# Optimization experiments

Hardware: AMD Instinct MI355X
Metric: run time of the kernel (lower is better)

Reference implementation:

```python
import jax, jax.numpy as jnp
import numpy as np
import math


def setup_inputs() -> dict:
    key = jax.random.key(0)
    ks = jax.random.split(key, 8)
    B, C, H, W = 8, 512, 48, 48
    Cq = C // 8
    s = 0.05
    return {
        "x": jax.random.normal(ks[0], (B, C, H, W), jnp.float32),
        "Wq": jax.random.normal(ks[1], (Cq, C), jnp.float32) * s,
        "bq": jax.random.normal(ks[2], (Cq,), jnp.float32) * s,
        "Wk": jax.random.normal(ks[3], (Cq, C), jnp.float32) * s,
        "bk": jax.random.normal(ks[4], (Cq,), jnp.float32) * s,
        "Wv": jax.random.normal(ks[5], (C, C), jnp.float32) * s,
        "bv": jax.random.normal(ks[6], (C,), jnp.float32) * s,
        "gamma": jax.random.normal(ks[7], (1,), jnp.float32),
    }


def reference(x, Wq, bq, Wk, bk, Wv, bv, gamma):
    B, C, H, W = x.shape
    Cq = Wq.shape[0]
    N = H * W
    xf = x.reshape(B, C, N)  # 1x1 conv == channel matmul
    q = jnp.einsum('oc,bcn->bno', Wq, xf) + bq  # [B, N, Cq] (proj_query, permuted)
    k = jnp.einsum('oc,bcn->bon', Wk, xf) + bk[None, :, None]  # [B, Cq, N]
    v = jnp.einsum('oc,bcn->bon', Wv, xf) + bv[None, :, None]  # [B, C, N]
    # ave_I = (1/Cq)*(I - (1/Cq)*J); Q @ ave_I = (Q - rowmean(Q)) / Cq
    qc = (q - jnp.mean(q, axis=-1, keepdims=True)) / Cq
    sigma = jnp.einsum('bnc,bcm->bnm', qc, k) / math.sqrt(Cq)  # [B, N, N]
    attention = jax.nn.softmax(sigma, axis=-1)
    # out = V @ attention^T : out[b,c,n] = sum_m v[b,c,m] * attention[b,n,m]
    am = jnp.einsum('bcm,bnm->bcn', v, attention).reshape(B, C, H, W)
    out = gamma[0] * am + x
    return out
```

## Files before the change

### kernel.cpp

```cpp
#include <hip/hip_runtime.h>

#define B_ 8
#define C_ 512
#define N_ 2304
#define CQ 64

typedef float f32x2 __attribute__((ext_vector_type(2)));
typedef float f32x4 __attribute__((ext_vector_type(4)));
typedef float f32x16 __attribute__((ext_vector_type(16)));
typedef short bf16x8 __attribute__((ext_vector_type(8)));
typedef unsigned short u16x4 __attribute__((ext_vector_type(4)));
typedef unsigned short u16x8 __attribute__((ext_vector_type(8)));
typedef int i32x4 __attribute__((ext_vector_type(4)));

__device__ __forceinline__ unsigned short f2bf(float f){
  union { float f; unsigned int u; } v; v.f = f;
  unsigned int r = (v.u + 0x7fffu + ((v.u >> 16) & 1u)) >> 16;
  return (unsigned short)r;
}

__device__ __forceinline__ void gload_lds16(const void* g, void* l){
  __builtin_amdgcn_global_load_lds(
      (const __attribute__((address_space(1))) unsigned int*)g,
      (__attribute__((address_space(3))) unsigned int*)l, 16, 0, 0);
}

__device__ __forceinline__ void fp8q_to_bf16(int w0, int w1, bf16x8* o){
  f32x2 a = __builtin_amdgcn_cvt_pk_f32_fp8(w0, false);
  f32x2 b = __builtin_amdgcn_cvt_pk_f32_fp8(w0, true);
  f32x2 c = __builtin_amdgcn_cvt_pk_f32_fp8(w1, false);
  f32x2 d = __builtin_amdgcn_cvt_pk_f32_fp8(w1, true);
  unsigned int u0,u1,u2,u3;
  asm("v_cvt_pk_bf16_f32 %0, %1, %2" : "=v"(u0) : "v"(a[0]), "v"(a[1]));
  asm("v_cvt_pk_bf16_f32 %0, %1, %2" : "=v"(u1) : "v"(b[0]), "v"(b[1]));
  asm("v_cvt_pk_bf16_f32 %0, %1, %2" : "=v"(u2) : "v"(c[0]), "v"(c[1]));
  asm("v_cvt_pk_bf16_f32 %0, %1, %2" : "=v"(u3) : "v"(d[0]), "v"(d[1]));
  union { unsigned int u[4]; bf16x8 v; } r;
  r.u[0]=u0; r.u[1]=u1; r.u[2]=u2; r.u[3]=u3;
  *o = r.v;
}

__global__ __launch_bounds__(256) void k_wcvt(const float* __restrict__ Wq,
                                              const float* __restrict__ Wk,
                                              const float* __restrict__ Wv,
                                              unsigned short* __restrict__ Wb){
  int idx = blockIdx.x*256 + threadIdx.x;
  int h = idx & 1, ln = (idx >> 1) & 31, cs = (idx >> 6) & 31, ob = idx >> 11;
  int row = ob*32 + ln, col = cs*16 + h*8;
  const float* src;
  if (row < 64)       src = Wq + (size_t)row*512 + col;
  else if (row < 128) src = Wk + (size_t)(row-64)*512 + col;
  else                src = Wv + (size_t)(row-128)*512 + col;
  f32x4 v0 = *(const f32x4*)src;
  f32x4 v1 = *(const f32x4*)(src + 4);
  u16x8 o;
  #pragma unroll
  for (int j = 0; j < 4; j++){ o[j] = f2bf(v0[j]); o[4+j] = f2bf(v1[j]); }
  *(u16x8*)(Wb + (size_t)idx*8) = o;
}

__global__ __launch_bounds__(512) void k_prep(const float* __restrict__ x,
                                              const float* __restrict__ bq,
                                              const float* __restrict__ bk,
                                              const float* __restrict__ bv,
                                              const unsigned short* __restrict__ Wb,
                                              unsigned short* __restrict__ qw,
                                              unsigned short* __restrict__ kw,
                                              unsigned short* __restrict__ vw){
  __shared__ short xt_l[32*520];
  __shared__ float scr[2*32*68];

  int i = blockIdx.x; int b = i & 7; int nt = i >> 3;
  int n0 = nt*32;
  int t = threadIdx.x; int w = t >> 6; int l = t & 63;
  int h = l >> 5, ln = l & 31;
  const size_t bN = (size_t)b*N_;

  #pragma unroll
  for (int it = 0; it < 8; it++){
    int c = it*64 + (t >> 3);
    int n4 = (t & 7)*4;
    f32x4 v = *(const f32x4*)(x + ((size_t)b*C_ + c)*N_ + n0 + n4);
    #pragma unroll
    for (int j = 0; j < 4; j++) xt_l[(n4+j)*520 + c] = (short)f2bf(v[j]);
  }
  __syncthreads();

  const unsigned short* wlane = Wb + (size_t)(ln*2 + h)*8;
  const unsigned short* wv0 = wlane + (size_t)(4 + 2*w)*16384;
  const unsigned short* wv1 = wlane + (size_t)(5 + 2*w)*16384;
  const unsigned short* wqk = wlane + (size_t)w*16384;

  f32x16 vacc[2]; f32x16 qkacc;
  #pragma unroll
  for (int rr = 0; rr < 16; rr++){ vacc[0][rr]=0.f; vacc[1][rr]=0.f; qkacc[rr]=0.f; }

  #pragma unroll 8
  for (int cs = 0; cs < 32; cs++){
    bf16x8 bx = *(const bf16x8*)&xt_l[ln*520 + cs*16 + h*8];
    bf16x8 a0 = *(const bf16x8*)(wv0 + (size_t)cs*512);
    bf16x8 a1 = *(const bf16x8*)(wv1 + (size_t)cs*512);
    vacc[0] = __builtin_amdgcn_mfma_f32_32x32x16_bf16(a0, bx, vacc[0], 0, 0, 0);
    vacc[1] = __builtin_amdgcn_mfma_f32_32x32x16_bf16(a1, bx, vacc[1], 0, 0, 0);
    if (w < 4){
      bf16x8 aq = *(const bf16x8*)(wqk + (size_t)cs*512);
      qkacc = __builtin_amdgcn_mfma_f32_32x32x16_bf16(aq, bx, qkacc, 0, 0, 0);
    }
  }

  if (w < 4){
    float* s = scr + ((w >> 1) ? 2176 : 0);
    int obase = (w & 1)*32;
    #pragma unroll
    for (int rr = 0; rr < 16; rr++){
      int o = obase + (rr & 3) + 8*(rr >> 2) + 4*h;
      s[ln*68 + o] = qkacc[rr];
    }
  }
  __syncthreads();

  if (t < 256){
    int isK = t >> 7;
    int tt = t & 127;
    int n = tt >> 2, j = tt & 3;
    const float* s = scr + (isK ? 2176 : 0);
    const float* bias = isK ? bk : bq;
    float vals[16]; float sm = 0.f;
    #pragma unroll
    for (int ii = 0; ii < 16; ii++){
      vals[ii] = s[n*68 + j*16 + ii] + bias[j*16 + ii];
      sm += vals[ii];
    }
    sm += __shfl_xor(sm, 1); sm += __shfl_xor(sm, 2);
    float mean = isK ? 0.f : sm * (1.f/64.f);
    float scl  = isK ? 1.f : (1.44269504089f/512.f);
    u16x8 h0, h1;
    #pragma unroll
    for (int ii = 0; ii < 8; ii++) h0[ii] = f2bf((vals[ii]   - mean)*scl);
    #pragma unroll
    for (int ii = 0; ii < 8; ii++) h1[ii] = f2bf((vals[8+ii] - mean)*scl);
    unsigned short* d = (isK ? kw : qw) + (bN + n0 + n)*CQ + j*16;
    *(u16x8*)d = h0;
    *(u16x8*)(d + 8) = h1;
  }
  __syncthreads();

  #pragma unroll
  for (int r = 0; r < 4; r++){
    if ((w >> 1) == r){
      float* s = scr + (w & 1)*2176;
      #pragma unroll
      for (int of = 0; of < 2; of++)
        #pragma unroll
        for (int rr = 0; rr < 16; rr++){
          int o = of*32 + (rr & 3) + 8*(rr >> 2) + 4*h;
          s[ln*68 + o] = vacc[of][rr];
        }
    }
    __syncthreads();
    {
      int ch = t >> 8;
      int tt = t & 255;
      int o = tt >> 2, jj = (tt >> 1) & 1, half = tt & 1;
      int og = (2*r + ch)*64 + o;
      const float* s = scr + ch*2176;
      float bvv = bv[og];
      u16x8 hv;
      #pragma unroll
      for (int ii = 0; ii < 8; ii++){
        int q2 = ((ii & 3) | ((ii & 4) << 1)) + half*4;
        hv[ii] = f2bf(s[(jj*16 + q2)*68 + o] + bvv);
      }
      *(u16x8*)(vw + ((size_t)b*C_ + og)*N_ + n0 + jj*16 + half*8) = hv;
    }
    __syncthreads();
  }
}

__global__ __launch_bounds__(256) void k_sexp(const unsigned short* __restrict__ qw,
                                              const unsigned short* __restrict__ kw,
                                              unsigned char* __restrict__ Plf,
                                              float* __restrict__ lsum_part,
                                              int b0, int bsh){
  int bid = blockIdx.x;
  int bl = bid & ((1 << bsh) - 1);
  int b = b0 + bl;
  int r = bid >> bsh;
  int ms = r & 3; int nt = r >> 2;
  int t = threadIdx.x; int w = t >> 6; int l = t & 63;
  int h = l >> 5, ln = l & 31;
  int nf = w & 1, mh = w >> 1;
  int n = nt*64 + nf*32 + ln;

  const unsigned short* qb = qw + ((size_t)b*N_ + n)*CQ + h*8;
  bf16x8 qf[4];
  #pragma unroll
  for (int kq = 0; kq < 4; kq++) qf[kq] = *(const bf16x8*)(qb + kq*16);

  int mb32base = ms*18 + mh*9;
  const unsigned short* ks0 = kw + ((size_t)b*N_ + ln)*CQ + h*8 + (size_t)mb32base*32*CQ;
  unsigned char* pbf = Plf + (((size_t)bl*72*N_ + n)*32) + h*16;

  float lsum = 0.f;
  bf16x8 ka[4], kc[4];
  #pragma unroll
  for (int kq = 0; kq < 4; kq++) ka[kq] = *(const bf16x8*)(ks0 + kq*16);

  #define SEXP_BODY(MF, KF, KN, PFOFF)                                          \
  {                                                                             \
    _Pragma("unroll")                                                           \
    for (int kq = 0; kq < 4; kq++)                                              \
      KN[kq] = *(const bf16x8*)(ks0 + (size_t)(PFOFF)*32*CQ + kq*16);           \
    f32x16 sv;                                                                  \
    _Pragma("unroll")                                                           \
    for (int rr = 0; rr < 16; rr++) sv[rr] = 0.f;                               \
    _Pragma("unroll")                                                           \
    for (int kq = 0; kq < 4; kq++)                                              \
      sv = __builtin_amdgcn_mfma_f32_32x32x16_bf16(KF[kq], qf[kq], sv, 0, 0, 0);\
    float e[16];                                                                \
    _Pragma("unroll")                                                           \
    for (int rr = 0; rr < 16; rr++) e[rr] = exp2f(sv[rr]);                      \
    _Pragma("unroll")                                                           \
    for (int rr = 0; rr < 16; rr++) lsum += e[rr];                              \
    int w0 = __builtin_amdgcn_cvt_pk_fp8_f32(e[0],  e[1],  0,  false);          \
    w0     = __builtin_amdgcn_cvt_pk_fp8_f32(e[2],  e[3],  w0, true);           \
    int w1 = __builtin_amdgcn_cvt_pk_fp8_f32(e[4],  e[5],  0,  false);          \
    w1     = __builtin_amdgcn_cvt_pk_fp8_f32(e[6],  e[7],  w1, true);           \
    int w2 = __builtin_amdgcn_cvt_pk_fp8_f32(e[8],  e[9],  0,  false);          \
    w2     = __builtin_amdgcn_cvt_pk_fp8_f32(e[10], e[11], w2, true);           \
    int w3 = __builtin_amdgcn_cvt_pk_fp8_f32(e[12], e[13], 0,  false);          \
    w3     = __builtin_amdgcn_cvt_pk_fp8_f32(e[14], e[15], w3, true);           \
    i32x4 pk4 = (i32x4){w0, w1, w2, w3};                                        \
    *(i32x4*)(pbf + (size_t)(mb32base + (MF))*((size_t)N_*32)) = pk4;           \
  }

  #pragma unroll
  for (int it = 0; it < 4; it++){
    SEXP_BODY(2*it,     ka, kc, 2*it + 1)
    SEXP_BODY(2*it + 1, kc, ka, 2*it + 2)
  }
  SEXP_BODY(8, ka, kc, 8)
  #undef SEXP_BODY

  lsum += __shfl_xor(lsum, 32);
  if (l < 32)
    lsum_part[((size_t)bl*8 + ms*2 + mh)*N_ + n] = lsum;
}

__global__ __launch_bounds__(256, 1) void k_pv(const unsigned short* __restrict__ vw,
                                               const unsigned char* __restrict__ Plf,
                                               const float* __restrict__ lsum_part,
                                               const float* __restrict__ x,
                                               const float* __restrict__ gamma_p,
                                               float* __restrict__ out,
                                               int b0, int bsh){
  __shared__ __attribute__((aligned(16))) short At[3][128*64];

  int bid = blockIdx.x;
  int bl = bid & ((1 << bsh) - 1);
  int b = b0 + bl;
  int r = bid >> bsh;
  int cb = r & 3; int nb = r >> 2;
  int c0 = cb*128, n0g = nb*64;
  int t = threadIdx.x; int w = t >> 6; int l = t & 63;
  int h = l >> 5, ln = l & 31;
  int wc = w & 1, wn = w >> 1;

  int gc = ((l & 7) - (l >> 3)) & 7;
  const unsigned short* asrc0 = vw + ((size_t)b*C_ + c0 + w*32 + (l >> 3))*N_ + gc*8;
  int aro[2][4];
  #pragma unroll
  for (int cf = 0; cf < 2; cf++)
    #pragma unroll
    for (int mb = 0; mb < 4; mb++){
      int row = wc*64 + cf*32 + ln;
      aro[cf][mb] = (row*8 + ((mb*2 + h + row) & 7)) * 16;
    }
  const unsigned char* Pbf = Plf + (size_t)bl*72*N_*32;
  size_t pstep = (size_t)N_*32;
  size_t boffB = (size_t)(n0g + wn*32 + ln)*32 + h*16;

  f32x16 acc[2];
  #pragma unroll
  for (int cf = 0; cf < 2; cf++)
    #pragma unroll
    for (int rr = 0; rr < 16; rr++) acc[cf][rr] = 0.f;

  i32x4 B0[2], B1[2], B2[2];

  #pragma unroll
  for (int j = 0; j < 4; j++)
    gload_lds16(asrc0 + (size_t)j*8*N_, &At[0][w*2048 + j*512]);
  B0[0] = *(const i32x4*)(Pbf + boffB);
  B0[1] = *(const i32x4*)(Pbf + pstep + boffB);
  #pragma unroll
  for (int j = 0; j < 4; j++)
    gload_lds16(asrc0 + (size_t)j*8*N_ + 64, &At[1][w*2048 + j*512]);
  B1[0] = *(const i32x4*)(Pbf + 2*pstep + boffB);
  B1[1] = *(const i32x4*)(Pbf + 3*pstep + boffB);
  asm volatile("s_waitcnt vmcnt(8)" ::: "memory");
  __builtin_amdgcn_s_barrier();
  __builtin_amdgcn_sched_barrier(0);

  #define PV_STEP(KT, RD, WR, BC, BN)                                           \
  {                                                                             \
    const char* Ab = (const char*)At[RD];                                       \
    bf16x8 a_[2][4];                                                            \
    _Pragma("unroll")                                                           \
    for (int cf = 0; cf < 2; cf++)                                              \
      _Pragma("unroll")                                                         \
      for (int mb = 0; mb < 4; mb++)                                            \
        a_[cf][mb] = *(const bf16x8*)(Ab + aro[cf][mb]);                        \
    int m2 = ((KT) + 2 < 36) ? ((KT) + 2)*64 : 0;                               \
    _Pragma("unroll")                                                           \
    for (int j = 0; j < 4; j++)                                                 \
      gload_lds16(asrc0 + (size_t)j*8*N_ + m2, &At[WR][w*2048 + j*512]);        \
    {                                                                           \
      size_t pr2 = (size_t)((((KT) + 2 < 36) ? ((KT) + 2)*2 : 0));              \
      BN[0] = *(const i32x4*)(Pbf + pr2*pstep + boffB);                         \
      BN[1] = *(const i32x4*)(Pbf + (pr2 + 1)*pstep + boffB);                   \
    }                                                                           \
    bf16x8 bfr[4];                                                              \
    fp8q_to_bf16(BC[0][0], BC[0][1], &bfr[0]);                                  \
    fp8q_to_bf16(BC[0][2], BC[0][3], &bfr[1]);                                  \
    fp8q_to_bf16(BC[1][0], BC[1][1], &bfr[2]);                                  \
    fp8q_to_bf16(BC[1][2], BC[1][3], &bfr[3]);                                  \
    _Pragma("unroll")                                                           \
    for (int cf = 0; cf < 2; cf++)                                              \
      _Pragma("unroll")                                                         \
      for (int mb = 0; mb < 4; mb++)                                            \
        acc[cf] = __builtin_amdgcn_mfma_f32_32x32x16_bf16(                      \
            a_[cf][mb], bfr[mb], acc[cf], 0, 0, 0);                             \
    asm volatile("s_waitcnt vmcnt(8) lgkmcnt(0)" ::: "memory");                 \
    __builtin_amdgcn_s_barrier();                                               \
    __builtin_amdgcn_sched_barrier(0);                                          \
  }

  for (int it = 0; it < 6; it++){
    int kt = it*6;
    PV_STEP(kt+0, 0, 2, B0, B2)
    PV_STEP(kt+1, 1, 0, B1, B0)
    PV_STEP(kt+2, 2, 1, B2, B1)
    PV_STEP(kt+3, 0, 2, B0, B2)
    PV_STEP(kt+4, 1, 0, B1, B0)
    PV_STEP(kt+5, 2, 1, B2, B1)
  }
  #undef PV_STEP

  float gmv = gamma_p[0];
  {
    int n = n0g + wn*32 + ln;
    float s = 0.f;
    #pragma unroll
    for (int j = 0; j < 8; j++) s += lsum_part[((size_t)bl*8 + j)*N_ + n];
    float f = gmv / s;
    #pragma unroll
    for (int cf = 0; cf < 2; cf++){
      #pragma unroll
      for (int rr = 0; rr < 16; rr++){
        int c = c0 + wc*64 + cf*32 + (rr & 3) + 8*(rr >> 2) + 4*h;
        size_t idx = ((size_t)b*C_ + c)*N_ + n;
        out[idx] = acc[cf][rr]*f + x[idx];
      }
    }
  }
}

extern "C" void kernel_launch(void* const* d_in, const int* in_sizes, int n_in,
                              void* d_out, int out_size, void* d_ws, size_t ws_size,
                              hipStream_t stream) {
  (void)in_sizes; (void)n_in; (void)out_size;
  const float* x  = (const float*)d_in[0];
  const float* Wq = (const float*)d_in[1];
  const float* bq = (const float*)d_in[2];
  const float* Wk = (const float*)d_in[3];
  const float* bk = (const float*)d_in[4];
  const float* Wv = (const float*)d_in[5];
  const float* bv = (const float*)d_in[6];
  const float* gm = (const float*)d_in[7];
  float* out = (float*)d_out;

  const size_t qw_b = (size_t)B_*N_*CQ*2;
  const size_t vw_b = (size_t)B_*C_*N_*2;
  const size_t wb_b = (size_t)640*512*2;

  int nbg = 8, bsh = 3;
  for (;;){
    size_t pl_b   = (size_t)nbg*72*N_*32;
    size_t lsum_b = (size_t)nbg*8*N_*4;
    size_t need   = pl_b + 2*qw_b + vw_b + lsum_b + wb_b;
    if (need <= ws_size || nbg == 1) break;
    nbg >>= 1; bsh--;
  }
  size_t pl_b   = (size_t)nbg*72*N_*32;
  size_t lsum_b = (size_t)nbg*8*N_*4;

  char* wsc = (char*)d_ws;
  unsigned char* Plf = (unsigned char*)wsc;
  unsigned short* qw = (unsigned short*)(wsc + pl_b);
  unsigned short* kw = (unsigned short*)(wsc + pl_b + qw_b);
  unsigned short* vw = (unsigned short*)(wsc + pl_b + 2*qw_b);
  float* lsum_part   = (float*)(wsc + pl_b + 2*qw_b + vw_b);
  unsigned short* Wb = (unsigned short*)(wsc + pl_b + 2*qw_b + vw_b + lsum_b);

  k_wcvt<<<160, 256, 0, stream>>>(Wq, Wk, Wv, Wb);
  k_prep<<<576, 512, 0, stream>>>(x, bq, bk, bv, Wb, qw, kw, vw);

  for (int b0 = 0; b0 < B_; b0 += nbg){
    k_sexp<<<144*nbg, 256, 0, stream>>>(qw, kw, Plf, lsum_part, b0, bsh);
    k_pv<<<144*nbg, 256, 0, stream>>>(vw, Plf, lsum_part, x, gm, out, b0, bsh);
  }
}
```

Before: 121.4 us.

## Store V in fp8 and use fp8×fp8 MFMA for the PV product

```diff
diff --git a/kernel.cpp b/kernel.cpp
--- a/kernel.cpp
+++ b/kernel.cpp
@@ -11,6 +11,7 @@
 typedef short bf16x8 __attribute__((ext_vector_type(8)));
 typedef unsigned short u16x4 __attribute__((ext_vector_type(4)));
 typedef unsigned short u16x8 __attribute__((ext_vector_type(8)));
+typedef int i32x2 __attribute__((ext_vector_type(2)));
 typedef int i32x4 __attribute__((ext_vector_type(4)));
 
 __device__ __forceinline__ unsigned short f2bf(float f){
@@ -23,21 +24,6 @@
   __builtin_amdgcn_global_load_lds(
       (const __attribute__((address_space(1))) unsigned int*)g,
       (__attribute__((address_space(3))) unsigned int*)l, 16, 0, 0);
-}
-
-__device__ __forceinline__ void fp8q_to_bf16(int w0, int w1, bf16x8* o){
-  f32x2 a = __builtin_amdgcn_cvt_pk_f32_fp8(w0, false);
-  f32x2 b = __builtin_amdgcn_cvt_pk_f32_fp8(w0, true);
-  f32x2 c = __builtin_amdgcn_cvt_pk_f32_fp8(w1, false);
-  f32x2 d = __builtin_amdgcn_cvt_pk_f32_fp8(w1, true);
-  unsigned int u0,u1,u2,u3;
-  asm("v_cvt_pk_bf16_f32 %0, %1, %2" : "=v"(u0) : "v"(a[0]), "v"(a[1]));
-  asm("v_cvt_pk_bf16_f32 %0, %1, %2" : "=v"(u1) : "v"(b[0]), "v"(b[1]));
-  asm("v_cvt_pk_bf16_f32 %0, %1, %2" : "=v"(u2) : "v"(c[0]), "v"(c[1]));
-  asm("v_cvt_pk_bf16_f32 %0, %1, %2" : "=v"(u3) : "v"(d[0]), "v"(d[1]));
-  union { unsigned int u[4]; bf16x8 v; } r;
-  r.u[0]=u0; r.u[1]=u1; r.u[2]=u2; r.u[3]=u3;
-  *o = r.v;
 }
 
 __global__ __launch_bounds__(256) void k_wcvt(const float* __restrict__ Wq,
@@ -66,7 +52,7 @@
                                               const unsigned short* __restrict__ Wb,
                                               unsigned short* __restrict__ qw,
                                               unsigned short* __restrict__ kw,
-                                              unsigned short* __restrict__ vw){
+                                              unsigned char* __restrict__ vw8){
   __shared__ short xt_l[32*520];
   __shared__ float scr[2*32*68];
 
@@ -165,13 +151,18 @@
       int og = (2*r + ch)*64 + o;
       const float* s = scr + ch*2176;
       float bvv = bv[og];
-      u16x8 hv;
+      float vv[8];
       #pragma unroll
       for (int ii = 0; ii < 8; ii++){
         int q2 = ((ii & 3) | ((ii & 4) << 1)) + half*4;
-        hv[ii] = f2bf(s[(jj*16 + q2)*68 + o] + bvv);
+        vv[ii] = s[(jj*16 + q2)*68 + o] + bvv;
       }
-      *(u16x8*)(vw + ((size_t)b*C_ + og)*N_ + n0 + jj*16 + half*8) = hv;
+      int w0 = __builtin_amdgcn_cvt_pk_fp8_f32(vv[0], vv[1], 0,  false);
+      w0     = __builtin_amdgcn_cvt_pk_fp8_f32(vv[2], vv[3], w0, true);
+      int w1 = __builtin_amdgcn_cvt_pk_fp8_f32(vv[4], vv[5], 0,  false);
+      w1     = __builtin_amdgcn_cvt_pk_fp8_f32(vv[6], vv[7], w1, true);
+      size_t dst = ((size_t)b*C_ + og)*N_ + n0 + jj*16 + half*8;
+      *(i32x2*)(vw8 + dst) = (i32x2){w0, w1};
     }
     __syncthreads();
   }
@@ -247,14 +238,14 @@
     lsum_part[((size_t)bl*8 + ms*2 + mh)*N_ + n] = lsum;
 }
 
-__global__ __launch_bounds__(256, 1) void k_pv(const unsigned short* __restrict__ vw,
+__global__ __launch_bounds__(256, 1) void k_pv(const unsigned char* __restrict__ vw8,
                                                const unsigned char* __restrict__ Plf,
                                                const float* __restrict__ lsum_part,
                                                const float* __restrict__ x,
                                                const float* __restrict__ gamma_p,
                                                float* __restrict__ out,
                                                int b0, int bsh){
-  __shared__ __attribute__((aligned(16))) short At[3][128*64];
+  __shared__ __attribute__((aligned(16))) char At[3][8192];
 
   int bid = blockIdx.x;
   int bl = bid & ((1 << bsh) - 1);
@@ -266,15 +257,25 @@
   int h = l >> 5, ln = l & 31;
   int wc = w & 1, wn = w >> 1;
 
-  int gc = ((l & 7) - (l >> 3)) & 7;
-  const unsigned short* asrc0 = vw + ((size_t)b*C_ + c0 + w*32 + (l >> 3))*N_ + gc*8;
+  const unsigned char* asrc[2];
+  int adst[2];
+  #pragma unroll
+  for (int j = 0; j < 2; j++){
+    int row = j*64 + (t >> 2);
+    int pos = t & 3;
+    int f = (row + (row >> 2)) & 3;
+    int q = (pos - f) & 3;
+    asrc[j] = vw8 + ((size_t)b*C_ + c0 + row)*N_ + q*16;
+    adst[j] = j*4096 + w*1024;
+  }
   int aro[2][4];
   #pragma unroll
   for (int cf = 0; cf < 2; cf++)
     #pragma unroll
     for (int mb = 0; mb < 4; mb++){
       int row = wc*64 + cf*32 + ln;
-      aro[cf][mb] = (row*8 + ((mb*2 + h + row) & 7)) * 16;
+      int f = (row + (row >> 2)) & 3;
+      aro[cf][mb] = row*64 + ((mb + f) & 3)*16 + h*8;
     }
   const unsigned char* Pbf = Plf + (size_t)bl*72*N_*32;
   size_t pstep = (size_t)N_*32;
@@ -286,52 +287,48 @@
     #pragma unroll
     for (int rr = 0; rr < 16; rr++) acc[cf][rr] = 0.f;
 
-  i32x4 B0[2], B1[2], B2[2];
-
-  #pragma unroll
-  for (int j = 0; j < 4; j++)
-    gload_lds16(asrc0 + (size_t)j*8*N_, &At[0][w*2048 + j*512]);
-  B0[0] = *(const i32x4*)(Pbf + boffB);
-  B0[1] = *(const i32x4*)(Pbf + pstep + boffB);
-  #pragma unroll
-  for (int j = 0; j < 4; j++)
-    gload_lds16(asrc0 + (size_t)j*8*N_ + 64, &At[1][w*2048 + j*512]);
-  B1[0] = *(const i32x4*)(Pbf + 2*pstep + boffB);
-  B1[1] = *(const i32x4*)(Pbf + 3*pstep + boffB);
-  asm volatile("s_waitcnt vmcnt(8)" ::: "memory");
+  union bu { i32x4 v; long lg[2]; };
+  bu B0[2], B1[2], B2[2];
+
+  #pragma unroll
+  for (int j = 0; j < 2; j++)
+    gload_lds16(asrc[j], At[0] + adst[j]);
+  B0[0].v = *(const i32x4*)(Pbf + boffB);
+  B0[1].v = *(const i32x4*)(Pbf + pstep + boffB);
+  #pragma unroll
+  for (int j = 0; j < 2; j++)
+    gload_lds16(asrc[j] + 64, At[1] + adst[j]);
+  B1[0].v = *(const i32x4*)(Pbf + 2*pstep + boffB);
+  B1[1].v = *(const i32x4*)(Pbf + 3*pstep + boffB);
+  asm volatile("s_waitcnt vmcnt(6)" ::: "memory");
   __builtin_amdgcn_s_barrier();
   __builtin_amdgcn_sched_barrier(0);
 
   #define PV_STEP(KT, RD, WR, BC, BN)                                           \
   {                                                                             \
     const char* Ab = (const char*)At[RD];                                       \
-    bf16x8 a_[2][4];                                                            \
+    long a_[2][4];                                                              \
     _Pragma("unroll")                                                           \
     for (int cf = 0; cf < 2; cf++)                                              \
       _Pragma("unroll")                                                         \
       for (int mb = 0; mb < 4; mb++)                                            \
-        a_[cf][mb] = *(const bf16x8*)(Ab + aro[cf][mb]);                        \
+        a_[cf][mb] = *(const long*)(Ab + aro[cf][mb]);                          \
     int m2 = ((KT) + 2 < 36) ? ((KT) + 2)*64 : 0;                               \
     _Pragma("unroll")                                                           \
-    for (int j = 0; j < 4; j++)                                                 \
-      gload_lds16(asrc0 + (size_t)j*8*N_ + m2, &At[WR][w*2048 + j*512]);        \
+    for (int j = 0; j < 2; j++)                                                 \
+      gload_lds16(asrc[j] + m2, At[WR] + adst[j]);                              \
     {                                                                           \
       size_t pr2 = (size_t)((((KT) + 2 < 36) ? ((KT) + 2)*2 : 0));              \
-      BN[0] = *(const i32x4*)(Pbf + pr2*pstep + boffB);                         \
-      BN[1] = *(const i32x4*)(Pbf + (pr2 + 1)*pstep + boffB);                   \
+      BN[0].v = *(const i32x4*)(Pbf + pr2*pstep + boffB);                       \
+      BN[1].v = *(const i32x4*)(Pbf + (pr2 + 1)*pstep + boffB);                 \
     }                                                                           \
-    bf16x8 bfr[4];                                                              \
-    fp8q_to_bf16(BC[0][0], BC[0][1], &bfr[0]);                                  \
-    fp8q_to_bf16(BC[0][2], BC[0][3], &bfr[1]);                                  \
-    fp8q_to_bf16(BC[1][0], BC[1][1], &bfr[2]);                                  \
-    fp8q_to_bf16(BC[1][2], BC[1][3], &bfr[3]);                                  \
     _Pragma("unroll")                                                           \
     for (int cf = 0; cf < 2; cf++)                                              \
       _Pragma("unroll")                                                         \
       for (int mb = 0; mb < 4; mb++)                                            \
-        acc[cf] = __builtin_amdgcn_mfma_f32_32x32x16_bf16(                      \
-            a_[cf][mb], bfr[mb], acc[cf], 0, 0, 0);                             \
-    asm volatile("s_waitcnt vmcnt(8) lgkmcnt(0)" ::: "memory");                 \
+        acc[cf] = __builtin_amdgcn_mfma_f32_32x32x16_fp8_fp8(                   \
+            a_[cf][mb], BC[mb >> 1].lg[mb & 1], acc[cf], 0, 0, 0);              \
+    asm volatile("s_waitcnt vmcnt(6) lgkmcnt(0)" ::: "memory");                 \
     __builtin_amdgcn_s_barrier();                                               \
     __builtin_amdgcn_sched_barrier(0);                                          \
   }
@@ -381,7 +378,7 @@
   float* out = (float*)d_out;
 
   const size_t qw_b = (size_t)B_*N_*CQ*2;
-  const size_t vw_b = (size_t)B_*C_*N_*2;
+  const size_t vw_b = (size_t)B_*C_*N_;
   const size_t wb_b = (size_t)640*512*2;
 
   int nbg = 8, bsh = 3;
@@ -399,15 +396,15 @@
   unsigned char* Plf = (unsigned char*)wsc;
   unsigned short* qw = (unsigned short*)(wsc + pl_b);
   unsigned short* kw = (unsigned short*)(wsc + pl_b + qw_b);
-  unsigned short* vw = (unsigned short*)(wsc + pl_b + 2*qw_b);
+  unsigned char* vw8 = (unsigned char*)(wsc + pl_b + 2*qw_b);
   float* lsum_part   = (float*)(wsc + pl_b + 2*qw_b + vw_b);
   unsigned short* Wb = (unsigned short*)(wsc + pl_b + 2*qw_b + vw_b + lsum_b);
 
   k_wcvt<<<160, 256, 0, stream>>>(Wq, Wk, Wv, Wb);
-  k_prep<<<576, 512, 0, stream>>>(x, bq, bk, bv, Wb, qw, kw, vw);
+  k_prep<<<576, 512, 0, stream>>>(x, bq, bk, bv, Wb, qw, kw, vw8);
 
   for (int b0 = 0; b0 < B_; b0 += nbg){
     k_sexp<<<144*nbg, 256, 0, stream>>>(qw, kw, Plf, lsum_part, b0, bsh);
-    k_pv<<<144*nbg, 256, 0, stream>>>(vw, Plf, lsum_part, x, gm, out, b0, bsh);
-  }
-}
+    k_pv<<<144*nbg, 256, 0, stream>>>(vw8, Plf, lsum_part, x, gm, out, b0, bsh);
+  }
+}
```

New measurement: 110.6 us, median of 2. 1.1x faster.
